# Kernel optimization log

Hardware: AMD Instinct MI355X
Metric: run time of the kernel (lower is better)

## Reference

```python
import jax, jax.numpy as jnp
import numpy as np

EMBED_DIM = 1024
BATCH = 4
SEQ = 2048


def setup_inputs() -> dict:
    key = jax.random.key(0)
    kx, kq, kk, kv = jax.random.split(key, 4)
    x = jax.random.normal(kx, (BATCH, SEQ, EMBED_DIM), dtype=jnp.float32)
    # nn.Linear weights are [out, in]; y = x @ W.T
    scale = 1.0 / np.sqrt(EMBED_DIM)
    Wq = jax.random.uniform(kq, (EMBED_DIM, EMBED_DIM), jnp.float32, -scale, scale)
    Wk = jax.random.uniform(kk, (EMBED_DIM, EMBED_DIM), jnp.float32, -scale, scale)
    Wv = jax.random.uniform(kv, (EMBED_DIM, EMBED_DIM), jnp.float32, -scale, scale)
    return {"x": x, "Wq": Wq, "Wk": Wk, "Wv": Wv}


def reference(x, Wq, Wk, Wv):
    # q/k/v projections (Linear without bias: x @ W.T)
    q = jnp.einsum("bse,fe->bsf", x, Wq)
    k = jnp.einsum("bse,fe->bsf", x, Wk)
    v = jnp.einsum("bse,fe->bsf", x, Wv)
    inv_sqrt_d = 1.0 / np.sqrt(x.shape[-1]).astype(np.float32)
    scores = jnp.einsum("bqf,bkf->bqk", q, k) * inv_sqrt_d  # [B, S, S]
    attn = jax.nn.softmax(scores, axis=-1)
    return jnp.einsum("bqk,bkf->bqf", attn, v)
```

## Files before the change

kernel.cpp:

```cpp
#include <hip/hip_runtime.h>
#include <stdint.h>

typedef unsigned short u16;
typedef __bf16 bf16x8 __attribute__((ext_vector_type(8)));
typedef float f32x4 __attribute__((ext_vector_type(4)));

__device__ __forceinline__ u16 f2bf(float f) {
    union { float f; uint32_t u; } c; c.f = f;
    return (u16)((c.u + 0x7fffu + ((c.u >> 16) & 1u)) >> 16);
}

__device__ __forceinline__ void g2lds16(const u16* g, u16* l) {
    __builtin_amdgcn_global_load_lds(
        (__attribute__((address_space(1))) void*)(void*)(g),
        (__attribute__((address_space(3))) void*)(l),
        16, 0, 0);
}


__global__ void cvt_f32_bf16(const float* __restrict__ in, u16* __restrict__ out, int n4) {
    int i = blockIdx.x * blockDim.x + threadIdx.x;
    int st = gridDim.x * blockDim.x;
    for (; i < n4; i += st) {
        float4 f = reinterpret_cast<const float4*>(in)[i];
        ushort4 u{ f2bf(f.x), f2bf(f.y), f2bf(f.z), f2bf(f.w) };
        reinterpret_cast<ushort4*>(out)[i] = u;
    }
}


template <int OUT_F32>
__global__ __launch_bounds__(512, 2)
void gemm256(const u16* __restrict__ A, const u16* __restrict__ B,
             void* __restrict__ Cv, int K, int lda, int ldb, int ldc,
             int bshift, size_t strideB, float scale)
{
    __shared__ __align__(16) u16 lds[4 * 16384];

    const int tid  = threadIdx.x;
    const int wid  = tid >> 6, lane = tid & 63;
    const int wr = wid >> 2, wc = wid & 3;
    const int row0 = blockIdx.y * 256;
    const int col0 = blockIdx.x * 256;
    const u16* Bb = B + (size_t)(row0 >> bshift) * strideB;

    int s_row[2], s_k[2], s_dst[2];
    #pragma unroll
    for (int c = 0; c < 2; ++c) {
        int p = c * 512 + tid;
        int line = p >> 3, ls = (p & 7) ^ (line & 7);
        s_row[c] = 2 * line + (ls >> 2);
        s_k[c]   = (ls & 3) * 8;
        s_dst[c] = (c * 512 + (tid & ~63)) * 8;
    }

    auto stageA = [&](int T) {
        const int sb = (T & 3) * 16384, k0 = T * 32;
        #pragma unroll
        for (int c = 0; c < 2; ++c)
            g2lds16(A + (size_t)(row0 + s_row[c]) * lda + k0 + s_k[c],
                    &lds[sb + s_dst[c]]);
    };
    auto stageB = [&](int T) {
        const int sb = (T & 3) * 16384, k0 = T * 32;
        #pragma unroll
        for (int c = 0; c < 2; ++c)
            g2lds16(Bb + (size_t)(col0 + s_row[c]) * ldb + k0 + s_k[c],
                    &lds[sb + 8192 + s_dst[c]]);
    };

    const int rl = lane & 15, kq = lane >> 4;
    const int ls = ((rl & 1) * 4 + kq) ^ ((rl >> 1) & 7);
    const int aoff = (wr * 64 + (rl >> 1)) * 64 + ls * 8;
    const int boff = 8192 + (wc * 32 + (rl >> 1)) * 64 + ls * 8;

    f32x4 acc[8][4] = {};
    bf16x8 afr[4], bfr[4];

    stageA(0); stageB(0); stageA(1); stageB(1); stageA(2); stageB(2);
    asm volatile("s_waitcnt vmcnt(8)" ::: "memory");
    __builtin_amdgcn_s_barrier();

    const int NT = K >> 5;
    for (int T = 0; T < NT; ++T) {
        const int sb = (T & 3) * 16384;

        #pragma unroll
        for (int m = 0; m < 4; ++m) afr[m] = *(const bf16x8*)&lds[sb + aoff + m * 512];
        #pragma unroll
        for (int n = 0; n < 4; ++n) bfr[n] = *(const bf16x8*)&lds[sb + boff + n * 512];
        if (T + 3 < NT) stageA(T + 3);
        __builtin_amdgcn_s_barrier();
        asm volatile("s_waitcnt lgkmcnt(0)" ::: "memory");
        __builtin_amdgcn_sched_barrier(0);
        __builtin_amdgcn_s_setprio(1);
        #pragma unroll
        for (int m = 0; m < 4; ++m)
            #pragma unroll
            for (int n = 0; n < 4; ++n)
                acc[m][n] = __builtin_amdgcn_mfma_f32_16x16x32_bf16(afr[m], bfr[n], acc[m][n], 0, 0, 0);
        __builtin_amdgcn_s_setprio(0);
        __builtin_amdgcn_s_barrier();

        #pragma unroll
        for (int m = 0; m < 4; ++m) afr[m] = *(const bf16x8*)&lds[sb + aoff + (m + 4) * 512];
        if (T + 3 < NT) stageB(T + 3);
        if (T < NT - 3)       { asm volatile("s_waitcnt vmcnt(8)" ::: "memory"); }
        else if (T == NT - 3) { asm volatile("s_waitcnt vmcnt(4)" ::: "memory"); }
        else if (T == NT - 2) { asm volatile("s_waitcnt vmcnt(0)" ::: "memory"); }
        __builtin_amdgcn_s_barrier();
        asm volatile("s_waitcnt lgkmcnt(0)" ::: "memory");
        __builtin_amdgcn_sched_barrier(0);
        __builtin_amdgcn_s_setprio(1);
        #pragma unroll
        for (int m = 0; m < 4; ++m)
            #pragma unroll
            for (int n = 0; n < 4; ++n)
                acc[m + 4][n] = __builtin_amdgcn_mfma_f32_16x16x32_bf16(afr[m], bfr[n], acc[m + 4][n], 0, 0, 0);
        __builtin_amdgcn_s_setprio(0);
        __builtin_amdgcn_s_barrier();
    }

    const int crow = row0 + wr * 128 + (lane >> 4) * 4;
    const int ccol = col0 + wc * 64 + (lane & 15);
    if constexpr (OUT_F32) {
        float* C = (float*)Cv;
        #pragma unroll
        for (int m = 0; m < 8; ++m)
            #pragma unroll
            for (int j = 0; j < 4; ++j) {
                size_t r = (size_t)(crow + m * 16 + j) * ldc;
                #pragma unroll
                for (int n = 0; n < 4; ++n)
                    C[r + ccol + n * 16] = acc[m][n][j] * scale;
            }
    } else {
        u16* C = (u16*)Cv;
        #pragma unroll
        for (int m = 0; m < 8; ++m)
            #pragma unroll
            for (int j = 0; j < 4; ++j) {
                size_t r = (size_t)(crow + m * 16 + j) * ldc;
                #pragma unroll
                for (int n = 0; n < 4; ++n)
                    C[r + ccol + n * 16] = f2bf(acc[m][n][j]);
            }
    }
}


__global__ __launch_bounds__(256)
void transpose_v(const u16* __restrict__ src, u16* __restrict__ dst) {
    __shared__ u16 t[64][72];
    const int tid = threadIdx.x;
    const int s0 = blockIdx.x * 64, f0 = blockIdx.y * 64;
    const int r = tid >> 3, c8 = (tid & 7) * 8;
    #pragma unroll
    for (int p = 0; p < 2; ++p) {
        const u16* s = &src[(size_t)(s0 + p * 32 + r) * 3072 + f0 + c8];
        ushort4 a = *(const ushort4*)s;
        ushort4 b = *(const ushort4*)(s + 4);
        *(ushort4*)&t[p * 32 + r][c8]     = a;
        *(ushort4*)&t[p * 32 + r][c8 + 4] = b;
    }
    __syncthreads();
    #pragma unroll
    for (int p = 0; p < 2; ++p) {
        int f = p * 32 + (tid >> 3);
        int sl = (tid & 7) * 8;
        ushort4 a{ t[sl + 0][f], t[sl + 1][f], t[sl + 2][f], t[sl + 3][f] };
        ushort4 b{ t[sl + 4][f], t[sl + 5][f], t[sl + 6][f], t[sl + 7][f] };
        u16* d = &dst[(size_t)(f0 + f) * 8192 + s0 + sl];
        *(ushort4*)d       = a;
        *(ushort4*)(d + 4) = b;
    }
}


__global__ __launch_bounds__(256)
void softmax_bf16(float* __restrict__ scores) {
    const size_t row = blockIdx.x;
    float* rp = scores + row * 2048;
    const int tid = threadIdx.x;
    const int lane = tid & 63, wid = tid >> 6;

    float4 a = reinterpret_cast<const float4*>(rp)[tid * 2];
    float4 b = reinterpret_cast<const float4*>(rp)[tid * 2 + 1];
    float v[8] = { a.x, a.y, a.z, a.w, b.x, b.y, b.z, b.w };

    float mx = v[0];
    #pragma unroll
    for (int j = 1; j < 8; ++j) mx = fmaxf(mx, v[j]);
    #pragma unroll
    for (int off = 32; off >= 1; off >>= 1) mx = fmaxf(mx, __shfl_xor(mx, off));

    __shared__ float red_mx[4], red_s[4];
    if (lane == 0) red_mx[wid] = mx;
    __syncthreads();
    mx = fmaxf(fmaxf(red_mx[0], red_mx[1]), fmaxf(red_mx[2], red_mx[3]));

    float s = 0.f;
    #pragma unroll
    for (int j = 0; j < 8; ++j) { v[j] = __expf(v[j] - mx); s += v[j]; }
    #pragma unroll
    for (int off = 32; off >= 1; off >>= 1) s += __shfl_xor(s, off);
    if (lane == 0) red_s[wid] = s;
    __syncthreads();
    s = (red_s[0] + red_s[1]) + (red_s[2] + red_s[3]);
    float inv = 1.0f / s;

    u16* pw = (u16*)rp;
    ushort4 u0{ f2bf(v[0] * inv), f2bf(v[1] * inv), f2bf(v[2] * inv), f2bf(v[3] * inv) };
    ushort4 u1{ f2bf(v[4] * inv), f2bf(v[5] * inv), f2bf(v[6] * inv), f2bf(v[7] * inv) };
    reinterpret_cast<ushort4*>(pw)[tid * 2]     = u0;
    reinterpret_cast<ushort4*>(pw)[tid * 2 + 1] = u1;
}


extern "C" void kernel_launch(void* const* d_in, const int* in_sizes, int n_in,
                              void* d_out, int out_size, void* d_ws, size_t ws_size,
                              hipStream_t stream) {
    const float* x  = (const float*)d_in[0];
    const float* Wq = (const float*)d_in[1];
    const float* Wk = (const float*)d_in[2];
    const float* Wv = (const float*)d_in[3];

    const size_t MiB = 1024 * 1024;
    if (ws_size < 128 * MiB) return;
    char* base = (char*)d_ws;
    float* sc   = (float*)base;
    u16*  xb    = (u16*)base;
    u16*  Wqkvb = (u16*)(base + 16 * MiB);
    u16*  qkvb  = (u16*)(base + 64 * MiB);
    u16*  vT    = (u16*)(base + 112 * MiB);

    cvt_f32_bf16<<<2048, 256, 0, stream>>>(x,  xb, 8192 * 1024 / 4);
    cvt_f32_bf16<<<1024, 256, 0, stream>>>(Wq, Wqkvb,               1024 * 1024 / 4);
    cvt_f32_bf16<<<1024, 256, 0, stream>>>(Wk, Wqkvb + 1024 * 1024, 1024 * 1024 / 4);
    cvt_f32_bf16<<<1024, 256, 0, stream>>>(Wv, Wqkvb + 2048 * 1024, 1024 * 1024 / 4);

    gemm256<0><<<dim3(12, 32), 512, 0, stream>>>(xb, Wqkvb, qkvb,
        1024, 1024, 1024, 3072, 31, 0, 1.0f);

    transpose_v<<<dim3(128, 16), 256, 0, stream>>>(qkvb + 2048, vT);

    gemm256<1><<<dim3(8, 32), 512, 0, stream>>>(qkvb, qkvb + 1024, sc,
        1024, 3072, 3072, 2048, 11, (size_t)2048 * 3072, 0.03125f);

    softmax_bf16<<<8192, 256, 0, stream>>>(sc);

    gemm256<1><<<dim3(4, 32), 512, 0, stream>>>((const u16*)sc, vT, d_out,
        2048, 4096, 8192, 1024, 11, 2048, 1.0f);
}
```

Measured before the change: 214.6 us.

## Fuse V transpose into QKV GEMM epilogue, merge conversions, narrow PV tile

The four f32->bf16 conversion launches become a single kernel. The standalone V-transpose kernel is removed: the QKV GEMM epilogue now stages accumulators through LDS and writes V directly in transposed layout, while Q/K go out as coalesced ushort4 stores. The final attn@V GEMM uses a 256x128 tile (NWC=2) to double its grid from 128 to 256 blocks. This cuts launches and a full pass over V in global memory, at the cost of a more complex epilogue, extra LDS traffic, and more B reloads for the narrower tile.

```diff
diff --git a/kernel.cpp b/kernel.cpp
--- a/kernel.cpp
+++ b/kernel.cpp
@@ -2,8 +2,10 @@
 #include <stdint.h>
 
 typedef unsigned short u16;
+typedef uint32_t u32;
 typedef __bf16 bf16x8 __attribute__((ext_vector_type(8)));
 typedef float f32x4 __attribute__((ext_vector_type(4)));
+typedef uint32_t u32x4 __attribute__((ext_vector_type(4)));
 
 __device__ __forceinline__ u16 f2bf(float f) {
     union { float f; uint32_t u; } c; c.f = f;
@@ -17,31 +19,58 @@
         16, 0, 0);
 }
 
-
-__global__ void cvt_f32_bf16(const float* __restrict__ in, u16* __restrict__ out, int n4) {
-    int i = blockIdx.x * blockDim.x + threadIdx.x;
-    int st = gridDim.x * blockDim.x;
-    for (; i < n4; i += st) {
-        float4 f = reinterpret_cast<const float4*>(in)[i];
+template <int N> __device__ __forceinline__ void waitcnt_vm() {
+    if constexpr      (N == 8) asm volatile("s_waitcnt vmcnt(8)" ::: "memory");
+    else if constexpr (N == 6) asm volatile("s_waitcnt vmcnt(6)" ::: "memory");
+    else if constexpr (N == 4) asm volatile("s_waitcnt vmcnt(4)" ::: "memory");
+    else if constexpr (N == 3) asm volatile("s_waitcnt vmcnt(3)" ::: "memory");
+    else                       asm volatile("s_waitcnt vmcnt(0)" ::: "memory");
+}
+
+
+__global__ __launch_bounds__(256)
+void cvt_all(const float* __restrict__ x, const float* __restrict__ wq,
+             const float* __restrict__ wk, const float* __restrict__ wv,
+             u16* __restrict__ xb, u16* __restrict__ wb) {
+    const int b = blockIdx.x, tid = threadIdx.x;
+    const float* src; u16* dst; int off;
+    if (b < 2048) { src = x; dst = xb; off = b * 1024; }
+    else {
+        int w = (b - 2048) >> 8;
+        src = (w == 0) ? wq : (w == 1) ? wk : wv;
+        dst = wb + (size_t)w * 1048576;
+        off = ((b - 2048) & 255) * 1024;
+    }
+    #pragma unroll
+    for (int k2 = 0; k2 < 4; ++k2) {
+        int i = off + k2 * 256 + tid;
+        float4 f = reinterpret_cast<const float4*>(src)[i];
         ushort4 u{ f2bf(f.x), f2bf(f.y), f2bf(f.z), f2bf(f.w) };
-        reinterpret_cast<ushort4*>(out)[i] = u;
-    }
-}
-
-
-template <int OUT_F32>
+        reinterpret_cast<ushort4*>(dst)[i] = u;
+    }
+}
+
+
+template <int MODE, int NWC>
 __global__ __launch_bounds__(512, 2)
 void gemm256(const u16* __restrict__ A, const u16* __restrict__ B,
-             void* __restrict__ Cv, int K, int lda, int ldb, int ldc,
+             void* __restrict__ Cv, u16* __restrict__ vTp,
+             int K, int lda, int ldb, int ldc,
              int bshift, size_t strideB, float scale)
 {
-    __shared__ __align__(16) u16 lds[4 * 16384];
+    constexpr int MACC = (NWC == 4) ? 8 : 4;
+    constexpr int PH   = MACC / 2;
+    constexpr int SLOT = 8192 + 2048 * NWC;
+    constexpr int SBC  = NWC / 2;
+    constexpr int L    = 2 + SBC;
+
+    __shared__ __align__(16) u16 lds[4 * SLOT];
 
     const int tid  = threadIdx.x;
     const int wid  = tid >> 6, lane = tid & 63;
-    const int wr = wid >> 2, wc = wid & 3;
+    const int wr = wid / NWC, wc = wid % NWC;
     const int row0 = blockIdx.y * 256;
-    const int col0 = blockIdx.x * 256;
+    const int col0 = blockIdx.x * (64 * NWC);
     const u16* Bb = B + (size_t)(row0 >> bshift) * strideB;
 
     int s_row[2], s_k[2], s_dst[2];
@@ -55,47 +84,47 @@
     }
 
     auto stageA = [&](int T) {
-        const int sb = (T & 3) * 16384, k0 = T * 32;
+        const int sb = (T & 3) * SLOT, k0 = T * 32;
         #pragma unroll
         for (int c = 0; c < 2; ++c)
             g2lds16(A + (size_t)(row0 + s_row[c]) * lda + k0 + s_k[c],
                     &lds[sb + s_dst[c]]);
     };
     auto stageB = [&](int T) {
-        const int sb = (T & 3) * 16384, k0 = T * 32;
-        #pragma unroll
-        for (int c = 0; c < 2; ++c)
+        const int sb = (T & 3) * SLOT, k0 = T * 32;
+        #pragma unroll
+        for (int c = 0; c < SBC; ++c)
             g2lds16(Bb + (size_t)(col0 + s_row[c]) * ldb + k0 + s_k[c],
                     &lds[sb + 8192 + s_dst[c]]);
     };
 
     const int rl = lane & 15, kq = lane >> 4;
-    const int ls = ((rl & 1) * 4 + kq) ^ ((rl >> 1) & 7);
-    const int aoff = (wr * 64 + (rl >> 1)) * 64 + ls * 8;
-    const int boff = 8192 + (wc * 32 + (rl >> 1)) * 64 + ls * 8;
-
-    f32x4 acc[8][4] = {};
-    bf16x8 afr[4], bfr[4];
+    const int ls2  = ((rl & 1) * 4 + kq) ^ ((rl >> 1) & 7);
+    const int aoff = (wr * (MACC * 8) + (rl >> 1)) * 64 + ls2 * 8;
+    const int boff = 8192 + (wc * 32 + (rl >> 1)) * 64 + ls2 * 8;
+
+    f32x4 acc[MACC][4] = {};
+    bf16x8 afr[PH], bfr[4];
 
     stageA(0); stageB(0); stageA(1); stageB(1); stageA(2); stageB(2);
-    asm volatile("s_waitcnt vmcnt(8)" ::: "memory");
+    waitcnt_vm<2 * L>();
     __builtin_amdgcn_s_barrier();
 
     const int NT = K >> 5;
     for (int T = 0; T < NT; ++T) {
-        const int sb = (T & 3) * 16384;
-
-        #pragma unroll
-        for (int m = 0; m < 4; ++m) afr[m] = *(const bf16x8*)&lds[sb + aoff + m * 512];
-        #pragma unroll
-        for (int n = 0; n < 4; ++n) bfr[n] = *(const bf16x8*)&lds[sb + boff + n * 512];
+        const int sb = (T & 3) * SLOT;
+
+        #pragma unroll
+        for (int m = 0; m < PH; ++m) afr[m] = *(const bf16x8*)&lds[sb + aoff + m * 512];
+        #pragma unroll
+        for (int n = 0; n < 4; ++n)  bfr[n] = *(const bf16x8*)&lds[sb + boff + n * 512];
         if (T + 3 < NT) stageA(T + 3);
         __builtin_amdgcn_s_barrier();
         asm volatile("s_waitcnt lgkmcnt(0)" ::: "memory");
         __builtin_amdgcn_sched_barrier(0);
         __builtin_amdgcn_s_setprio(1);
         #pragma unroll
-        for (int m = 0; m < 4; ++m)
+        for (int m = 0; m < PH; ++m)
             #pragma unroll
             for (int n = 0; n < 4; ++n)
                 acc[m][n] = __builtin_amdgcn_mfma_f32_16x16x32_bf16(afr[m], bfr[n], acc[m][n], 0, 0, 0);
@@ -103,76 +132,86 @@
         __builtin_amdgcn_s_barrier();
 
         #pragma unroll
-        for (int m = 0; m < 4; ++m) afr[m] = *(const bf16x8*)&lds[sb + aoff + (m + 4) * 512];
+        for (int m = 0; m < PH; ++m) afr[m] = *(const bf16x8*)&lds[sb + aoff + (m + PH) * 512];
         if (T + 3 < NT) stageB(T + 3);
-        if (T < NT - 3)       { asm volatile("s_waitcnt vmcnt(8)" ::: "memory"); }
-        else if (T == NT - 3) { asm volatile("s_waitcnt vmcnt(4)" ::: "memory"); }
-        else if (T == NT - 2) { asm volatile("s_waitcnt vmcnt(0)" ::: "memory"); }
+        if (T < NT - 3)       waitcnt_vm<2 * L>();
+        else if (T == NT - 3) waitcnt_vm<L>();
+        else if (T == NT - 2) waitcnt_vm<0>();
         __builtin_amdgcn_s_barrier();
         asm volatile("s_waitcnt lgkmcnt(0)" ::: "memory");
         __builtin_amdgcn_sched_barrier(0);
         __builtin_amdgcn_s_setprio(1);
         #pragma unroll
-        for (int m = 0; m < 4; ++m)
+        for (int m = 0; m < PH; ++m)
             #pragma unroll
             for (int n = 0; n < 4; ++n)
-                acc[m + 4][n] = __builtin_amdgcn_mfma_f32_16x16x32_bf16(afr[m], bfr[n], acc[m + 4][n], 0, 0, 0);
+                acc[m + PH][n] = __builtin_amdgcn_mfma_f32_16x16x32_bf16(afr[m], bfr[n], acc[m + PH][n], 0, 0, 0);
         __builtin_amdgcn_s_setprio(0);
         __builtin_amdgcn_s_barrier();
     }
 
-    const int crow = row0 + wr * 128 + (lane >> 4) * 4;
-    const int ccol = col0 + wc * 64 + (lane & 15);
-    if constexpr (OUT_F32) {
+    const int kq4 = kq * 4;
+
+    if constexpr (MODE == 1) {
         float* C = (float*)Cv;
         #pragma unroll
-        for (int m = 0; m < 8; ++m)
+        for (int m = 0; m < MACC; ++m)
             #pragma unroll
             for (int j = 0; j < 4; ++j) {
-                size_t r = (size_t)(crow + m * 16 + j) * ldc;
+                size_t r = (size_t)(row0 + wr * (MACC * 16) + m * 16 + kq4 + j) * ldc;
                 #pragma unroll
                 for (int n = 0; n < 4; ++n)
-                    C[r + ccol + n * 16] = acc[m][n][j] * scale;
+                    C[r + col0 + wc * 64 + n * 16 + rl] = acc[m][n][j] * scale;
             }
-    } else {
-        u16* C = (u16*)Cv;
-        #pragma unroll
-        for (int m = 0; m < 8; ++m)
-            #pragma unroll
-            for (int j = 0; j < 4; ++j) {
-                size_t r = (size_t)(crow + m * 16 + j) * ldc;
+    } else if (col0 < 2048) {
+        float* tw = (float*)&lds[(size_t)wid * 8192];
+        u16* Cq = (u16*)Cv;
+        #pragma unroll
+        for (int h = 0; h < 2; ++h) {
+            #pragma unroll
+            for (int mm = 0; mm < 4; ++mm)
                 #pragma unroll
                 for (int n = 0; n < 4; ++n)
-                    C[r + ccol + n * 16] = f2bf(acc[m][n][j]);
+                    #pragma unroll
+                    for (int j = 0; j < 4; ++j) {
+                        int rowl = mm * 16 + kq4 + j;
+                        int c2 = (rl + n * 16) ^ ((((rowl) >> 2) & 3) << 4);
+                        tw[rowl * 64 + c2] = acc[h * 4 + mm][n][j];
+                    }
+            #pragma unroll
+            for (int it = 0; it < 16; ++it) {
+                int rowr = it * 4 + kq;
+                int c2 = (rl * 4) ^ ((it & 3) << 4);
+                f32x4 v4 = *(const f32x4*)&tw[rowr * 64 + c2];
+                ushort4 u{ f2bf(v4[0]), f2bf(v4[1]), f2bf(v4[2]), f2bf(v4[3]) };
+                *(ushort4*)&Cq[(size_t)(row0 + wr * 128 + h * 64 + rowr) * ldc
+                               + col0 + wc * 64 + rl * 4] = u;
             }
-    }
-}
-
-
-__global__ __launch_bounds__(256)
-void transpose_v(const u16* __restrict__ src, u16* __restrict__ dst) {
-    __shared__ u16 t[64][72];
-    const int tid = threadIdx.x;
-    const int s0 = blockIdx.x * 64, f0 = blockIdx.y * 64;
-    const int r = tid >> 3, c8 = (tid & 7) * 8;
-    #pragma unroll
-    for (int p = 0; p < 2; ++p) {
-        const u16* s = &src[(size_t)(s0 + p * 32 + r) * 3072 + f0 + c8];
-        ushort4 a = *(const ushort4*)s;
-        ushort4 b = *(const ushort4*)(s + 4);
-        *(ushort4*)&t[p * 32 + r][c8]     = a;
-        *(ushort4*)&t[p * 32 + r][c8 + 4] = b;
-    }
-    __syncthreads();
-    #pragma unroll
-    for (int p = 0; p < 2; ++p) {
-        int f = p * 32 + (tid >> 3);
-        int sl = (tid & 7) * 8;
-        ushort4 a{ t[sl + 0][f], t[sl + 1][f], t[sl + 2][f], t[sl + 3][f] };
-        ushort4 b{ t[sl + 4][f], t[sl + 5][f], t[sl + 6][f], t[sl + 7][f] };
-        u16* d = &dst[(size_t)(f0 + f) * 8192 + s0 + sl];
-        *(ushort4*)d       = a;
-        *(ushort4*)(d + 4) = b;
+        }
+    } else {
+        u32* tv = (u32*)&lds[(size_t)wid * 8192];
+        const int s0  = row0 + wr * 128;
+        const int f0v = col0 - 2048 + wc * 64;
+        #pragma unroll
+        for (int m = 0; m < 8; ++m)
+            #pragma unroll
+            for (int n = 0; n < 4; ++n)
+                #pragma unroll
+                for (int j2 = 0; j2 < 2; ++j2) {
+                    int fl = rl + n * 16;
+                    int s2 = m * 8 + kq * 2 + j2;
+                    u32 pk = (u32)f2bf(acc[m][n][j2 * 2])
+                           | ((u32)f2bf(acc[m][n][j2 * 2 + 1]) << 16);
+                    tv[fl * 64 + (s2 ^ ((fl & 15) << 2))] = pk;
+                }
+        #pragma unroll
+        for (int it = 0; it < 16; ++it) {
+            int fr = it * 4 + (lane >> 4);
+            int ck = lane & 15;
+            int s2s = (ck * 4) ^ ((fr & 15) << 2);
+            u32x4 v4 = *(const u32x4*)&tv[fr * 64 + s2s];
+            *(u32x4*)&vTp[(size_t)(f0v + fr) * 8192 + s0 + ck * 8] = v4;
+        }
     }
 }
 
@@ -226,29 +265,24 @@
     const float* Wv = (const float*)d_in[3];
 
     const size_t MiB = 1024 * 1024;
-    if (ws_size < 128 * MiB) return;
+    if (ws_size < 112 * MiB) return;
     char* base = (char*)d_ws;
     float* sc   = (float*)base;
     u16*  xb    = (u16*)base;
     u16*  Wqkvb = (u16*)(base + 16 * MiB);
-    u16*  qkvb  = (u16*)(base + 64 * MiB);
-    u16*  vT    = (u16*)(base + 112 * MiB);
-
-    cvt_f32_bf16<<<2048, 256, 0, stream>>>(x,  xb, 8192 * 1024 / 4);
-    cvt_f32_bf16<<<1024, 256, 0, stream>>>(Wq, Wqkvb,               1024 * 1024 / 4);
-    cvt_f32_bf16<<<1024, 256, 0, stream>>>(Wk, Wqkvb + 1024 * 1024, 1024 * 1024 / 4);
-    cvt_f32_bf16<<<1024, 256, 0, stream>>>(Wv, Wqkvb + 2048 * 1024, 1024 * 1024 / 4);
-
-    gemm256<0><<<dim3(12, 32), 512, 0, stream>>>(xb, Wqkvb, qkvb,
-        1024, 1024, 1024, 3072, 31, 0, 1.0f);
-
-    transpose_v<<<dim3(128, 16), 256, 0, stream>>>(qkvb + 2048, vT);
-
-    gemm256<1><<<dim3(8, 32), 512, 0, stream>>>(qkvb, qkvb + 1024, sc,
-        1024, 3072, 3072, 2048, 11, (size_t)2048 * 3072, 0.03125f);
+    u16*  qkb   = (u16*)(base + 64 * MiB);
+    u16*  vT    = (u16*)(base + 96 * MiB);
+
+    cvt_all<<<2816, 256, 0, stream>>>(x, Wq, Wk, Wv, xb, Wqkvb);
+
+    gemm256<0, 4><<<dim3(12, 32), 512, 0, stream>>>(xb, Wqkvb, qkb, vT,
+        1024, 1024, 1024, 2048, 31, 0, 1.0f);
+
+    gemm256<1, 4><<<dim3(8, 32), 512, 0, stream>>>(qkb, qkb + 1024, sc, nullptr,
+        1024, 2048, 2048, 2048, 11, (size_t)2048 * 2048, 0.03125f);
 
     softmax_bf16<<<8192, 256, 0, stream>>>(sc);
 
-    gemm256<1><<<dim3(4, 32), 512, 0, stream>>>((const u16*)sc, vT, d_out,
+    gemm256<1, 2><<<dim3(8, 32), 512, 0, stream>>>((const u16*)sc, vT, d_out, nullptr,
         2048, 4096, 8192, 1024, 11, 2048, 1.0f);
 }
```

After: 190.3 us. 11.3% less time.
